# Performance work log

Hardware: AMD Instinct MI355X
Metric: run time of the kernel (lower is better)

## Reference

```python
import jax, jax.numpy as jnp
import numpy as np

B, N, H, O = 2, 512, 128, 32  # batch, n_particles, hidden_dim, obs_dim


def _linear_init(key, out_d, in_d):
    kw, kb = jax.random.split(key)
    s = 1.0 / np.sqrt(in_d)
    W = jax.random.uniform(kw, (out_d, in_d), minval=-s, maxval=s, dtype=jnp.float32)
    b = jax.random.uniform(kb, (out_d,), minval=-s, maxval=s, dtype=jnp.float32)
    return W, b


def setup_inputs() -> dict:
    key = jax.random.key(0)
    ks = jax.random.split(key, 8)
    z = jax.random.normal(ks[0], (B, N, H), dtype=jnp.float32)
    s_t = jax.random.normal(ks[1], (B, N, O), dtype=jnp.float32)
    W1, b1 = _linear_init(ks[2], H, 2 * H)   # relation_mlp layer 0
    W2, b2 = _linear_init(ks[3], H, H)       # relation_mlp layer 2
    Wq, bq = _linear_init(ks[4], H, H)       # query_proj
    Wk, bk = _linear_init(ks[5], H, O)       # key_proj
    W3, b3 = _linear_init(ks[6], H, H)       # aggregation_mlp layer 0
    W4, b4 = _linear_init(ks[7], H, H)       # aggregation_mlp layer 2
    return dict(z=z, s_t=s_t, W1=W1, b1=b1, W2=W2, b2=b2, Wq=Wq, bq=bq,
                Wk=Wk, bk=bk, W3=W3, b3=b3, W4=W4, b4=b4)


def reference(z, s_t, W1, b1, W2, b2, Wq, bq, Wk, bk, W3, b3, W4, b4):
    b_, n, h = z.shape
    # query depends only on i, key only on j (repeat in the original is redundant)
    q = z @ Wq.T + bq            # [B,N,H]
    k = s_t @ Wk.T + bk          # [B,N,H]
    scores = jnp.einsum('bih,bjh->bij', q, k) / (h ** 0.5)   # [B,N,N]
    eye = jnp.eye(n, dtype=bool)
    scores = jnp.where(eye, -jnp.inf, scores)
    attn = jax.nn.softmax(scores, axis=-1)                   # [B,N,N]
    # relation_mlp on concat(z_i, z_j): split first weight into i- and j- halves
    W1i, W1j = W1[:, :h], W1[:, h:]
    zi = z @ W1i.T               # [B,N,H]
    zj = z @ W1j.T               # [B,N,H]
    rel = jnp.tanh(zi[:, :, None, :] + zj[:, None, :, :] + b1) @ W2.T + b2  # [B,N,N,H]
    agg = jnp.einsum('bij,bijh->bih', attn, rel)             # weighted sum over j
    dz_dt = jnp.tanh(agg @ W3.T + b3) @ W4.T + b4
    return dz_dt
```

## Files before the change

### kernel.cpp

```cpp
#include <hip/hip_runtime.h>
#include <hip/hip_bf16.h>

#define NN 512
#define HH 128
#define OO 32

#define KL 2.8853900817779268f

__device__ __forceinline__ float vexp2(float x) {
    float r; asm("v_exp_f32 %0, %1" : "=v"(r) : "v"(x)); return r;
}
__device__ __forceinline__ float vrcp(float x) {
    float r; asm("v_rcp_f32 %0, %1" : "=v"(r) : "v"(x)); return r;
}
__device__ __forceinline__ float tanh_fast(float x) {
    float e = vexp2(KL * x);
    return 1.0f - 2.0f * vrcp(e + 1.0f);
}
__device__ __forceinline__ float waveRedMax(float v) {
#pragma unroll
    for (int off = 32; off > 0; off >>= 1) v = fmaxf(v, __shfl_xor(v, off, 64));
    return v;
}
__device__ __forceinline__ float waveRedSum(float v) {
#pragma unroll
    for (int off = 32; off > 0; off >>= 1) v += __shfl_xor(v, off, 64);
    return v;
}
__device__ __forceinline__ float red8(float v) {
    v += __shfl_xor(v, 1, 64); v += __shfl_xor(v, 2, 64); v += __shfl_xor(v, 4, 64);
    return v;
}
__device__ __forceinline__ float dot16(const float4* w, const float* x) {
    float a = 0;
#pragma unroll
    for (int i = 0; i < 4; i++) {
        float4 xv = *(const float4*)(x + i * 4);
        a = fmaf(xv.x, w[i].x, a); a = fmaf(xv.y, w[i].y, a);
        a = fmaf(xv.z, w[i].z, a); a = fmaf(xv.w, w[i].w, a);
    }
    return a;
}

__global__ __launch_bounds__(1024, 4) void prep_kernel(
    const float* __restrict__ z, const float* __restrict__ s_t,
    const float* __restrict__ W1, const float* __restrict__ b1,
    const float* __restrict__ Wq, const float* __restrict__ bq,
    const float* __restrict__ Wk, const float* __restrict__ bk,
    float* __restrict__ qP, float* __restrict__ cP,
    float* __restrict__ EzjG, float* __restrict__ kTG) {
    __shared__ float zrow[4][HH];
    __shared__ float srow[4][OO];
    int t = threadIdx.x;
    int bid = blockIdx.x;
    int r0 = bid * 4;
    if (t < 4 * HH) zrow[t >> 7][t & 127] = z[(size_t)r0 * HH + t];
    else if (t < 4 * HH + 4 * OO) {
        int u = t - 4 * HH;
        srow[u >> 5][u & 31] = s_t[(size_t)r0 * OO + u];
    }
    __syncthreads();

    int kq = t & 7, h = t >> 3;
    float vbq = bq[h], vb1 = b1[h], vbk = bk[h];
    float4 w[4];
    float a0, a1, a2, a3;

    {
        const float4* Wp = (const float4*)(Wq + (size_t)h * HH) + kq * 4;
#pragma unroll
        for (int i = 0; i < 4; i++) w[i] = Wp[i];
        a0 = red8(dot16(w, &zrow[0][kq * 16]));
        a1 = red8(dot16(w, &zrow[1][kq * 16]));
        a2 = red8(dot16(w, &zrow[2][kq * 16]));
        a3 = red8(dot16(w, &zrow[3][kq * 16]));
        if (kq == 0) {
            float* qp = qP + (size_t)bid * 512 + h * 4;
            qp[0] = a0 + vbq; qp[1] = a1 + vbq; qp[2] = a2 + vbq; qp[3] = a3 + vbq;
        }
    }
    {
        const float4* Wp = (const float4*)(W1 + (size_t)h * 2 * HH) + kq * 4;
#pragma unroll
        for (int i = 0; i < 4; i++) w[i] = Wp[i];
        a0 = red8(dot16(w, &zrow[0][kq * 16]));
        a1 = red8(dot16(w, &zrow[1][kq * 16]));
        a2 = red8(dot16(w, &zrow[2][kq * 16]));
        a3 = red8(dot16(w, &zrow[3][kq * 16]));
        if (kq == 0) {
            float* cp = cP + (size_t)bid * 512 + h * 4;
            cp[0] = vexp2(KL * (a0 + vb1)); cp[1] = vexp2(KL * (a1 + vb1));
            cp[2] = vexp2(KL * (a2 + vb1)); cp[3] = vexp2(KL * (a3 + vb1));
        }
    }
    {
        const float4* Wp = (const float4*)(W1 + (size_t)h * 2 * HH + HH) + kq * 4;
#pragma unroll
        for (int i = 0; i < 4; i++) w[i] = Wp[i];
        a0 = red8(dot16(w, &zrow[0][kq * 16]));
        a1 = red8(dot16(w, &zrow[1][kq * 16]));
        a2 = red8(dot16(w, &zrow[2][kq * 16]));
        a3 = red8(dot16(w, &zrow[3][kq * 16]));
        if (kq == 0) {
            EzjG[(size_t)(r0 + 0) * HH + h] = vexp2(KL * a0);
            EzjG[(size_t)(r0 + 1) * HH + h] = vexp2(KL * a1);
            EzjG[(size_t)(r0 + 2) * HH + h] = vexp2(KL * a2);
            EzjG[(size_t)(r0 + 3) * HH + h] = vexp2(KL * a3);
        }
    }
    {
        float4 wk = ((const float4*)(Wk + (size_t)h * OO))[kq];
        float4 s0 = *(const float4*)&srow[0][kq * 4];
        float4 s1 = *(const float4*)&srow[1][kq * 4];
        float4 s2 = *(const float4*)&srow[2][kq * 4];
        float4 s3 = *(const float4*)&srow[3][kq * 4];
        a0 = red8(s0.x * wk.x + s0.y * wk.y + s0.z * wk.z + s0.w * wk.w);
        a1 = red8(s1.x * wk.x + s1.y * wk.y + s1.z * wk.z + s1.w * wk.w);
        a2 = red8(s2.x * wk.x + s2.y * wk.y + s2.z * wk.z + s2.w * wk.w);
        a3 = red8(s3.x * wk.x + s3.y * wk.y + s3.z * wk.z + s3.w * wk.w);
        if (kq == 0) {
            int b = r0 >> 9, j0 = r0 & 511;
            float* kp = kTG + ((size_t)b * HH + h) * NN + j0;
            kp[0] = a0 + vbk; kp[1] = a1 + vbk; kp[2] = a2 + vbk; kp[3] = a3 + vbk;
        }
    }
}

__global__ __launch_bounds__(1024, 4) void fused_kernel(
    const float* __restrict__ qP, const float* __restrict__ kTG,
    const float* __restrict__ cP, const float* __restrict__ EzjG,
    const float* __restrict__ W2, const float* __restrict__ b2,
    const float* __restrict__ W3, const float* __restrict__ b3,
    const float* __restrict__ W4, const float* __restrict__ b4,
    float* __restrict__ out) {
    __shared__ float q4T[HH][4];
    __shared__ float c4T[HH][4];
    __shared__ float attnT[NN][4];
    __shared__ float buf[8192];
    __shared__ float UL[4][HH];
    __shared__ float aggL[4][HH];
    __shared__ float h1L[4][HH];
    __shared__ float redA[16], redB[16];

    float (*scp)[4][NN] = (float (*)[4][NN])buf;
    float (*part)[4][HH] = (float (*)[4][HH])buf;

    int t = threadIdx.x;
    int bid = blockIdx.x;
    int b = bid >> 7;
    int i0 = (bid & 127) * 4;
    int r0 = bid * 4;

    if (t < 512)       ((float*)q4T)[t] = qP[(size_t)bid * 512 + t];
    else               ((float*)c4T)[t - 512] = cP[(size_t)bid * 512 + (t - 512)];
    __syncthreads();

    {
        int j = t & 511, hs = t >> 9, h0 = hs * 64;
        const float* kb = kTG + ((size_t)b * HH + h0) * NN + j;
        float s0 = 0, s1 = 0, s2 = 0, s3 = 0;
#pragma unroll 8
        for (int hh = 0; hh < 64; hh++) {
            float kv = kb[(size_t)hh * NN];
            float4 qv = *(const float4*)q4T[h0 + hh];
            s0 = fmaf(qv.x, kv, s0); s1 = fmaf(qv.y, kv, s1);
            s2 = fmaf(qv.z, kv, s2); s3 = fmaf(qv.w, kv, s3);
        }
        scp[hs][0][j] = s0; scp[hs][1][j] = s1;
        scp[hs][2][j] = s2; scp[hs][3][j] = s3;
    }
    __syncthreads();

    {
        int rp = t >> 9, j = t & 511;
        int lr0 = rp * 2, lr1 = lr0 + 1;
        const float sc = 0.08838834764831845f;
        float s0 = (scp[0][lr0][j] + scp[1][lr0][j]) * sc;
        float s1 = (scp[0][lr1][j] + scp[1][lr1][j]) * sc;
        if (j == i0 + lr0) s0 = -1e30f;
        if (j == i0 + lr1) s1 = -1e30f;
        int lane = t & 63, w = t >> 6, wb = rp * 8;
        float m0 = waveRedMax(s0), m1 = waveRedMax(s1);
        if (lane == 0) { redA[w] = m0; redB[w] = m1; }
        __syncthreads();
        float mm0 = redA[wb], mm1 = redB[wb];
#pragma unroll
        for (int k = 1; k < 8; k++) { mm0 = fmaxf(mm0, redA[wb + k]); mm1 = fmaxf(mm1, redB[wb + k]); }
        float e0 = __expf(s0 - mm0), e1 = __expf(s1 - mm1);
        float p0 = waveRedSum(e0), p1 = waveRedSum(e1);
        __syncthreads();
        if (lane == 0) { redA[w] = p0; redB[w] = p1; }
        __syncthreads();
        float S0 = redA[wb], S1 = redB[wb];
#pragma unroll
        for (int k = 1; k < 8; k++) { S0 += redA[wb + k]; S1 += redB[wb + k]; }
        attnT[j][lr0] = e0 * __fdividef(1.0f, S0);
        attnT[j][lr1] = e1 * __fdividef(1.0f, S1);
    }
    __syncthreads();

    {
        int lane6 = t & 63, qs = t >> 6;
        int hp = lane6 * 2;
        float4 cA = *(const float4*)c4T[hp];
        float4 cB = *(const float4*)c4T[hp + 1];
        const float2* zb2 = (const float2*)(EzjG + (size_t)b * NN * HH) + lane6;
        float a0A = 0, a1A = 0, a2A = 0, a3A = 0;
        float a0B = 0, a1B = 0, a2B = 0, a3B = 0;
        int jb = qs * 32;
#pragma unroll 8
        for (int jj = 0; jj < 32; jj++) {
            int j = jb + jj;
            float2 E = zb2[(size_t)j * 64];
            float4 w = *(const float4*)attnT[j];
            a0A = fmaf(w.x, vrcp(fmaf(cA.x, E.x, 1.0f)), a0A);
            a1A = fmaf(w.y, vrcp(fmaf(cA.y, E.x, 1.0f)), a1A);
            a2A = fmaf(w.z, vrcp(fmaf(cA.z, E.x, 1.0f)), a2A);
            a3A = fmaf(w.w, vrcp(fmaf(cA.w, E.x, 1.0f)), a3A);
            a0B = fmaf(w.x, vrcp(fmaf(cB.x, E.y, 1.0f)), a0B);
            a1B = fmaf(w.y, vrcp(fmaf(cB.y, E.y, 1.0f)), a1B);
            a2B = fmaf(w.z, vrcp(fmaf(cB.z, E.y, 1.0f)), a2B);
            a3B = fmaf(w.w, vrcp(fmaf(cB.w, E.y, 1.0f)), a3B);
        }
        __syncthreads();
        *(float2*)&part[qs][0][hp] = make_float2(a0A, a0B);
        *(float2*)&part[qs][1][hp] = make_float2(a1A, a1B);
        *(float2*)&part[qs][2][hp] = make_float2(a2A, a2B);
        *(float2*)&part[qs][3][hp] = make_float2(a3A, a3B);
    }
    __syncthreads();
    if (t < 512) {
        int r = t >> 7, h = t & 127;
        float s = 0;
#pragma unroll
        for (int q = 0; q < 16; q++) s += part[q][r][h];
        UL[r][h] = fmaf(-2.0f, s, 1.0f);
    }
    __syncthreads();

    {
        int kq = t & 7, h = t >> 3;
        float vb2 = b2[h], vb3 = b3[h], vb4 = b4[h];
        float4 w[4];
        {
            const float4* Wp = (const float4*)(W2 + (size_t)h * HH) + kq * 4;
#pragma unroll
            for (int i = 0; i < 4; i++) w[i] = Wp[i];
            float a0 = red8(dot16(w, &UL[0][kq * 16]));
            float a1 = red8(dot16(w, &UL[1][kq * 16]));
            float a2 = red8(dot16(w, &UL[2][kq * 16]));
            float a3 = red8(dot16(w, &UL[3][kq * 16]));
            if (kq == 0) {
                aggL[0][h] = a0 + vb2; aggL[1][h] = a1 + vb2;
                aggL[2][h] = a2 + vb2; aggL[3][h] = a3 + vb2;
            }
        }
        __syncthreads();
        {
            const float4* Wp = (const float4*)(W3 + (size_t)h * HH) + kq * 4;
#pragma unroll
            for (int i = 0; i < 4; i++) w[i] = Wp[i];
            float a0 = red8(dot16(w, &aggL[0][kq * 16]));
            float a1 = red8(dot16(w, &aggL[1][kq * 16]));
            float a2 = red8(dot16(w, &aggL[2][kq * 16]));
            float a3 = red8(dot16(w, &aggL[3][kq * 16]));
            if (kq == 0) {
                h1L[0][h] = tanh_fast(a0 + vb3); h1L[1][h] = tanh_fast(a1 + vb3);
                h1L[2][h] = tanh_fast(a2 + vb3); h1L[3][h] = tanh_fast(a3 + vb3);
            }
        }
        __syncthreads();
        {
            const float4* Wp = (const float4*)(W4 + (size_t)h * HH) + kq * 4;
#pragma unroll
            for (int i = 0; i < 4; i++) w[i] = Wp[i];
            float a0 = red8(dot16(w, &h1L[0][kq * 16]));
            float a1 = red8(dot16(w, &h1L[1][kq * 16]));
            float a2 = red8(dot16(w, &h1L[2][kq * 16]));
            float a3 = red8(dot16(w, &h1L[3][kq * 16]));
            if (kq == 0) {
                out[(size_t)(r0 + 0) * HH + h] = a0 + vb4;
                out[(size_t)(r0 + 1) * HH + h] = a1 + vb4;
                out[(size_t)(r0 + 2) * HH + h] = a2 + vb4;
                out[(size_t)(r0 + 3) * HH + h] = a3 + vb4;
            }
        }
    }
}

extern "C" void kernel_launch(void* const* d_in, const int* in_sizes, int n_in,
                              void* d_out, int out_size, void* d_ws, size_t ws_size,
                              hipStream_t stream) {
    const float* z   = (const float*)d_in[0];
    const float* s_t = (const float*)d_in[1];
    const float* W1  = (const float*)d_in[2];
    const float* b1  = (const float*)d_in[3];
    const float* W2  = (const float*)d_in[4];
    const float* b2  = (const float*)d_in[5];
    const float* Wq  = (const float*)d_in[6];
    const float* bq  = (const float*)d_in[7];
    const float* Wk  = (const float*)d_in[8];
    const float* bk  = (const float*)d_in[9];
    const float* W3  = (const float*)d_in[10];
    const float* b3  = (const float*)d_in[11];
    const float* W4  = (const float*)d_in[12];
    const float* b4  = (const float*)d_in[13];
    float* out = (float*)d_out;

    float* ws  = (float*)d_ws;
    float* qP  = ws;
    float* kT  = ws + 131072;
    float* cP  = ws + 262144;
    float* Ezj = ws + 393216;

    hipLaunchKernelGGL(prep_kernel, dim3(256), dim3(1024), 0, stream,
                       z, s_t, W1, b1, Wq, bq, Wk, bk, qP, cP, Ezj, kT);
    hipLaunchKernelGGL(fused_kernel, dim3(256), dim3(1024), 0, stream,
                       qP, kT, cP, Ezj, W2, b2, W3, b3, W4, b4, out);
}
```

Before: 32.98 us.

## Merge prep and fused kernels into one launch with per-batch atomic barrier

Fuses the projection prep kernel into the main kernel, so q and c stay in shared memory and only kT and Ezj go through global memory. A per-batch atomic counter spin barrier, reset by a memset before each launch, waits until all 128 blocks of a batch have written their keys and Ezj. This removes a kernel launch and the round trip of qP/cP through global memory. In exchange it depends on all 256 blocks being resident at once (1024 threads, 4 blocks per CU), adds a memset node, and adds spin-wait latency.

```diff
diff --git a/kernel.cpp b/kernel.cpp
--- a/kernel.cpp
+++ b/kernel.cpp
@@ -42,97 +42,19 @@
     return a;
 }
 
-__global__ __launch_bounds__(1024, 4) void prep_kernel(
+__global__ __launch_bounds__(1024, 4) void ode_one(
     const float* __restrict__ z, const float* __restrict__ s_t,
     const float* __restrict__ W1, const float* __restrict__ b1,
+    const float* __restrict__ W2, const float* __restrict__ b2,
     const float* __restrict__ Wq, const float* __restrict__ bq,
     const float* __restrict__ Wk, const float* __restrict__ bk,
-    float* __restrict__ qP, float* __restrict__ cP,
-    float* __restrict__ EzjG, float* __restrict__ kTG) {
+    const float* __restrict__ W3, const float* __restrict__ b3,
+    const float* __restrict__ W4, const float* __restrict__ b4,
+    float* __restrict__ out,
+    float* __restrict__ kTG, float* __restrict__ EzjG, int* __restrict__ cnt) {
+
     __shared__ float zrow[4][HH];
     __shared__ float srow[4][OO];
-    int t = threadIdx.x;
-    int bid = blockIdx.x;
-    int r0 = bid * 4;
-    if (t < 4 * HH) zrow[t >> 7][t & 127] = z[(size_t)r0 * HH + t];
-    else if (t < 4 * HH + 4 * OO) {
-        int u = t - 4 * HH;
-        srow[u >> 5][u & 31] = s_t[(size_t)r0 * OO + u];
-    }
-    __syncthreads();
-
-    int kq = t & 7, h = t >> 3;
-    float vbq = bq[h], vb1 = b1[h], vbk = bk[h];
-    float4 w[4];
-    float a0, a1, a2, a3;
-
-    {
-        const float4* Wp = (const float4*)(Wq + (size_t)h * HH) + kq * 4;
-#pragma unroll
-        for (int i = 0; i < 4; i++) w[i] = Wp[i];
-        a0 = red8(dot16(w, &zrow[0][kq * 16]));
-        a1 = red8(dot16(w, &zrow[1][kq * 16]));
-        a2 = red8(dot16(w, &zrow[2][kq * 16]));
-        a3 = red8(dot16(w, &zrow[3][kq * 16]));
-        if (kq == 0) {
-            float* qp = qP + (size_t)bid * 512 + h * 4;
-            qp[0] = a0 + vbq; qp[1] = a1 + vbq; qp[2] = a2 + vbq; qp[3] = a3 + vbq;
-        }
-    }
-    {
-        const float4* Wp = (const float4*)(W1 + (size_t)h * 2 * HH) + kq * 4;
-#pragma unroll
-        for (int i = 0; i < 4; i++) w[i] = Wp[i];
-        a0 = red8(dot16(w, &zrow[0][kq * 16]));
-        a1 = red8(dot16(w, &zrow[1][kq * 16]));
-        a2 = red8(dot16(w, &zrow[2][kq * 16]));
-        a3 = red8(dot16(w, &zrow[3][kq * 16]));
-        if (kq == 0) {
-            float* cp = cP + (size_t)bid * 512 + h * 4;
-            cp[0] = vexp2(KL * (a0 + vb1)); cp[1] = vexp2(KL * (a1 + vb1));
-            cp[2] = vexp2(KL * (a2 + vb1)); cp[3] = vexp2(KL * (a3 + vb1));
-        }
-    }
-    {
-        const float4* Wp = (const float4*)(W1 + (size_t)h * 2 * HH + HH) + kq * 4;
-#pragma unroll
-        for (int i = 0; i < 4; i++) w[i] = Wp[i];
-        a0 = red8(dot16(w, &zrow[0][kq * 16]));
-        a1 = red8(dot16(w, &zrow[1][kq * 16]));
-        a2 = red8(dot16(w, &zrow[2][kq * 16]));
-        a3 = red8(dot16(w, &zrow[3][kq * 16]));
-        if (kq == 0) {
-            EzjG[(size_t)(r0 + 0) * HH + h] = vexp2(KL * a0);
-            EzjG[(size_t)(r0 + 1) * HH + h] = vexp2(KL * a1);
-            EzjG[(size_t)(r0 + 2) * HH + h] = vexp2(KL * a2);
-            EzjG[(size_t)(r0 + 3) * HH + h] = vexp2(KL * a3);
-        }
-    }
-    {
-        float4 wk = ((const float4*)(Wk + (size_t)h * OO))[kq];
-        float4 s0 = *(const float4*)&srow[0][kq * 4];
-        float4 s1 = *(const float4*)&srow[1][kq * 4];
-        float4 s2 = *(const float4*)&srow[2][kq * 4];
-        float4 s3 = *(const float4*)&srow[3][kq * 4];
-        a0 = red8(s0.x * wk.x + s0.y * wk.y + s0.z * wk.z + s0.w * wk.w);
-        a1 = red8(s1.x * wk.x + s1.y * wk.y + s1.z * wk.z + s1.w * wk.w);
-        a2 = red8(s2.x * wk.x + s2.y * wk.y + s2.z * wk.z + s2.w * wk.w);
-        a3 = red8(s3.x * wk.x + s3.y * wk.y + s3.z * wk.z + s3.w * wk.w);
-        if (kq == 0) {
-            int b = r0 >> 9, j0 = r0 & 511;
-            float* kp = kTG + ((size_t)b * HH + h) * NN + j0;
-            kp[0] = a0 + vbk; kp[1] = a1 + vbk; kp[2] = a2 + vbk; kp[3] = a3 + vbk;
-        }
-    }
-}
-
-__global__ __launch_bounds__(1024, 4) void fused_kernel(
-    const float* __restrict__ qP, const float* __restrict__ kTG,
-    const float* __restrict__ cP, const float* __restrict__ EzjG,
-    const float* __restrict__ W2, const float* __restrict__ b2,
-    const float* __restrict__ W3, const float* __restrict__ b3,
-    const float* __restrict__ W4, const float* __restrict__ b4,
-    float* __restrict__ out) {
     __shared__ float q4T[HH][4];
     __shared__ float c4T[HH][4];
     __shared__ float attnT[NN][4];
@@ -151,8 +73,85 @@
     int i0 = (bid & 127) * 4;
     int r0 = bid * 4;
 
-    if (t < 512)       ((float*)q4T)[t] = qP[(size_t)bid * 512 + t];
-    else               ((float*)c4T)[t - 512] = cP[(size_t)bid * 512 + (t - 512)];
+    if (t < 4 * HH) zrow[t >> 7][t & 127] = z[(size_t)r0 * HH + t];
+    else if (t < 4 * HH + 4 * OO) {
+        int u = t - 4 * HH;
+        srow[u >> 5][u & 31] = s_t[(size_t)r0 * OO + u];
+    }
+    __syncthreads();
+
+    {
+        int kq = t & 7, h = t >> 3;
+        float vbq = bq[h], vb1 = b1[h], vbk = bk[h];
+        float4 w[4];
+        float a0, a1, a2, a3;
+        {
+            const float4* Wp = (const float4*)(Wq + (size_t)h * HH) + kq * 4;
+#pragma unroll
+            for (int i = 0; i < 4; i++) w[i] = Wp[i];
+            a0 = red8(dot16(w, &zrow[0][kq * 16]));
+            a1 = red8(dot16(w, &zrow[1][kq * 16]));
+            a2 = red8(dot16(w, &zrow[2][kq * 16]));
+            a3 = red8(dot16(w, &zrow[3][kq * 16]));
+            if (kq == 0) {
+                q4T[h][0] = a0 + vbq; q4T[h][1] = a1 + vbq;
+                q4T[h][2] = a2 + vbq; q4T[h][3] = a3 + vbq;
+            }
+        }
+        {
+            const float4* Wp = (const float4*)(W1 + (size_t)h * 2 * HH) + kq * 4;
+#pragma unroll
+            for (int i = 0; i < 4; i++) w[i] = Wp[i];
+            a0 = red8(dot16(w, &zrow[0][kq * 16]));
+            a1 = red8(dot16(w, &zrow[1][kq * 16]));
+            a2 = red8(dot16(w, &zrow[2][kq * 16]));
+            a3 = red8(dot16(w, &zrow[3][kq * 16]));
+            if (kq == 0) {
+                c4T[h][0] = vexp2(KL * (a0 + vb1)); c4T[h][1] = vexp2(KL * (a1 + vb1));
+                c4T[h][2] = vexp2(KL * (a2 + vb1)); c4T[h][3] = vexp2(KL * (a3 + vb1));
+            }
+        }
+        {
+            const float4* Wp = (const float4*)(W1 + (size_t)h * 2 * HH + HH) + kq * 4;
+#pragma unroll
+            for (int i = 0; i < 4; i++) w[i] = Wp[i];
+            a0 = red8(dot16(w, &zrow[0][kq * 16]));
+            a1 = red8(dot16(w, &zrow[1][kq * 16]));
+            a2 = red8(dot16(w, &zrow[2][kq * 16]));
+            a3 = red8(dot16(w, &zrow[3][kq * 16]));
+            if (kq == 0) {
+                EzjG[(size_t)(r0 + 0) * HH + h] = vexp2(KL * a0);
+                EzjG[(size_t)(r0 + 1) * HH + h] = vexp2(KL * a1);
+                EzjG[(size_t)(r0 + 2) * HH + h] = vexp2(KL * a2);
+                EzjG[(size_t)(r0 + 3) * HH + h] = vexp2(KL * a3);
+            }
+        }
+        {
+            float4 wk = ((const float4*)(Wk + (size_t)h * OO))[kq];
+            float4 s0 = *(const float4*)&srow[0][kq * 4];
+            float4 s1 = *(const float4*)&srow[1][kq * 4];
+            float4 s2 = *(const float4*)&srow[2][kq * 4];
+            float4 s3 = *(const float4*)&srow[3][kq * 4];
+            a0 = red8(s0.x * wk.x + s0.y * wk.y + s0.z * wk.z + s0.w * wk.w);
+            a1 = red8(s1.x * wk.x + s1.y * wk.y + s1.z * wk.z + s1.w * wk.w);
+            a2 = red8(s2.x * wk.x + s2.y * wk.y + s2.z * wk.z + s2.w * wk.w);
+            a3 = red8(s3.x * wk.x + s3.y * wk.y + s3.z * wk.z + s3.w * wk.w);
+            if (kq == 0) {
+                float4 kv = make_float4(a0 + vbk, a1 + vbk, a2 + vbk, a3 + vbk);
+                *(float4*)(kTG + ((size_t)b * HH + h) * NN + i0) = kv;
+            }
+        }
+    }
+    __syncthreads();
+
+    if (t == 0) {
+        __threadfence();
+        atomicAdd(&cnt[b], 1);
+        while (__hip_atomic_load(&cnt[b], __ATOMIC_RELAXED, __HIP_MEMORY_SCOPE_AGENT) < 128) {
+            __builtin_amdgcn_s_sleep(2);
+        }
+        __threadfence();
+    }
     __syncthreads();
 
     {
@@ -308,13 +307,12 @@
     float* out = (float*)d_out;
 
     float* ws  = (float*)d_ws;
-    float* qP  = ws;
-    float* kT  = ws + 131072;
-    float* cP  = ws + 262144;
-    float* Ezj = ws + 393216;
-
-    hipLaunchKernelGGL(prep_kernel, dim3(256), dim3(1024), 0, stream,
-                       z, s_t, W1, b1, Wq, bq, Wk, bk, qP, cP, Ezj, kT);
-    hipLaunchKernelGGL(fused_kernel, dim3(256), dim3(1024), 0, stream,
-                       qP, kT, cP, Ezj, W2, b2, W3, b3, W4, b4, out);
-}
+    float* kT  = ws;
+    float* Ezj = ws + 131072;
+    int*   cnt = (int*)(ws + 262144);
+
+    hipMemsetAsync(cnt, 0, 2 * sizeof(int), stream);
+    hipLaunchKernelGGL(ode_one, dim3(256), dim3(1024), 0, stream,
+                       z, s_t, W1, b1, W2, b2, Wq, bq, Wk, bk, W3, b3, W4, b4,
+                       out, kT, Ezj, cnt);
+}
```

Measured after the change: 53.36 us. 1.62x slower.
